# Kernel optimization log

Measured on AMD Instinct MI355X. Metric: run time of the kernel, lower is better.

The kernel has to match this reference:

```python
import jax, jax.numpy as jnp
import numpy as np

B, L, F, H = 8, 1024, 1024, 16
D = F // H  # feat_head = 64
EPS = 1e-5


def setup_inputs() -> dict:
    key = jax.random.key(0)
    ks = jax.random.split(key, 12)
    s = 1.0 / np.sqrt(F)
    inp = {
        "q": jax.random.normal(ks[0], (B, L, F), jnp.float32),
        "k": jax.random.normal(ks[1], (B, L, F), jnp.float32),
        "v": jax.random.normal(ks[2], (B, L, F), jnp.float32),
        "Wq": jax.random.uniform(ks[3], (F, F), jnp.float32, -s, s),
        "bq": jax.random.uniform(ks[4], (F,), jnp.float32, -s, s),
        "Wk": jax.random.uniform(ks[5], (F, F), jnp.float32, -s, s),
        "bk": jax.random.uniform(ks[6], (F,), jnp.float32, -s, s),
        "Wv": jax.random.uniform(ks[7], (F, F), jnp.float32, -s, s),
        "bv": jax.random.uniform(ks[8], (F,), jnp.float32, -s, s),
        "Wf": jax.random.uniform(ks[9], (F, F), jnp.float32, -s, s),
        "bf": jax.random.uniform(ks[10], (F,), jnp.float32, -s, s),
        "gamma": jnp.ones((F,), jnp.float32),
        "beta": jnp.zeros((F,), jnp.float32),
    }
    return inp


def _split_heads(x):
    # (B, L, F) -> (B*H, L, D), matching reshape->transpose(1,2)->reshape
    return x.reshape(B, L, H, D).transpose(0, 2, 1, 3).reshape(B * H, L, D)


def reference(q, k, v, Wq, bq, Wk, bk, Wv, bv, Wf, bf, gamma, beta):
    residual = q
    qh = _split_heads(q @ Wq.T + bq)
    kh = _split_heads(k @ Wk.T + bk)
    vh = _split_heads(v @ Wv.T + bv)
    # scores: (B*H, L, L)
    scores = jnp.einsum('nqd,nkd->nqk', qh, kh) / np.sqrt(D)
    raw_att = jax.nn.softmax(scores, axis=-1)
    att = jnp.einsum('nqk,nkd->nqd', raw_att, vh)  # (B*H, L, D)
    # faithful to original output recombine: reshape(H, B, L, D).permute(1,2,0,3)
    att = att.reshape(H, B, L, D).transpose(1, 2, 0, 3).reshape(B, L, F)
    att = att @ Wf.T + bf
    # dropout in eval mode = identity; activation is None
    x = att + residual
    mu = jnp.mean(x, axis=-1, keepdims=True)
    var = jnp.mean(jnp.square(x - mu), axis=-1, keepdims=True)
    out = (x - mu) * jax.lax.rsqrt(var + EPS) * gamma + beta
    return out, raw_att
```

## Files before the change

### kernel.cpp

```cpp
#include <hip/hip_runtime.h>

#define BB 8
#define LL 1024
#define FF 1024
#define HH 16
#define DD 64
#define NBH 128

typedef __attribute__((ext_vector_type(8))) short bf16x8;
typedef __attribute__((ext_vector_type(4))) float f32x4;

#define GLD_LDS16(g, l)                                                        \
  __builtin_amdgcn_global_load_lds(                                            \
      (const __attribute__((address_space(1))) unsigned int*)(g),              \
      (__attribute__((address_space(3))) unsigned int*)(l), 16, 0, 0)

__device__ __forceinline__ unsigned short f2bf(float f) {
  unsigned int u = __float_as_uint(f);
  unsigned int r = u + 0x7fffu + ((u >> 16) & 1u);
  return (unsigned short)(r >> 16);
}

__global__ __launch_bounds__(256) void cvt3_kernel(const float* __restrict__ s0,
                                                   const float* __restrict__ s1,
                                                   const float* __restrict__ s2,
                                                   short* __restrict__ dst, int n4) {
  int z = blockIdx.y;
  const float* src = (z == 0) ? s0 : (z == 1) ? s1 : s2;
  int i = blockIdx.x * 256 + threadIdx.x;
  if (i >= n4) return;
  float4 v = ((const float4*)src)[i];
  short4 o;
  o.x = (short)f2bf(v.x); o.y = (short)f2bf(v.y);
  o.z = (short)f2bf(v.z); o.w = (short)f2bf(v.w);
  ((short4*)(dst + (size_t)z * n4 * 4))[i] = o;
}

__global__ __launch_bounds__(256) void cvt4_kernel(const float* __restrict__ s0,
                                                   const float* __restrict__ s1,
                                                   const float* __restrict__ s2,
                                                   const float* __restrict__ s3,
                                                   short* __restrict__ dst, int n4) {
  int z = blockIdx.y;
  const float* src = (z == 0) ? s0 : (z == 1) ? s1 : (z == 2) ? s2 : s3;
  int i = blockIdx.x * 256 + threadIdx.x;
  if (i >= n4) return;
  float4 v = ((const float4*)src)[i];
  short4 o;
  o.x = (short)f2bf(v.x); o.y = (short)f2bf(v.y);
  o.z = (short)f2bf(v.z); o.w = (short)f2bf(v.w);
  ((short4*)(dst + (size_t)z * n4 * 4))[i] = o;
}

__global__ __launch_bounds__(256) void proj_qkv(
    const short* __restrict__ Aall, const short* __restrict__ Wall,
    const float* __restrict__ bq, const float* __restrict__ bk,
    const float* __restrict__ bv, short* __restrict__ Dall) {
  const int o = blockIdx.x + (blockIdx.y << 6) + (blockIdx.z << 9);
  const int n = ((o & 7) * 192) + (o >> 3);
  const int z = n >> 9;
  const int r = n & 511;
  const int by = r & 7, bx = r >> 3;

  const short* A  = Aall + (size_t)z * (BB * LL * FF);
  const short* Bt = Wall + (size_t)z * (FF * FF);
  const float* bias = (z == 0) ? bq : (z == 1) ? bk : bv;
  short* dst = Dall + (size_t)z * ((size_t)NBH * LL * DD);
  const float scale = (z == 0) ? 0.125f * 1.44269504088896f : 1.0f;

  __shared__ __attribute__((aligned(16))) short LB[128 * 136];
  short* As = LB;
  short* Bs = LB + 128 * 64;

  const int tid = threadIdx.x;
  const int lane = tid & 63, w = tid >> 6;
  const int wr = w >> 1, wc = w & 1;
  const int row16 = lane & 15, kg = lane >> 4;
  const int m0 = bx * 128, n0 = by * 128;

  const f32x4 z4 = {0.f, 0.f, 0.f, 0.f};
  f32x4 acc[4][4];
  for (int i = 0; i < 4; ++i)
    for (int j = 0; j < 4; ++j) acc[i][j] = z4;

  for (int k0 = 0; k0 < FF; k0 += 64) {
#pragma unroll
    for (int rr = 0; rr < 4; ++rr) {
      int e8 = tid + rr * 256;
      int row = e8 >> 3, cs = ((e8 & 7) ^ (row & 7)) * 8;
      GLD_LDS16(A + (size_t)(m0 + row) * FF + k0 + cs, As + e8 * 8);
      GLD_LDS16(Bt + (size_t)(n0 + row) * FF + k0 + cs, Bs + e8 * 8);
    }
    __syncthreads();
#pragma unroll
    for (int kk2 = 0; kk2 < 2; ++kk2) {
      bf16x8 af[4], bfr[4];
#pragma unroll
      for (int i = 0; i < 4; ++i) {
        int ra = wr * 64 + i * 16 + row16;
        int rb = wc * 64 + i * 16 + row16;
        af[i]  = *(const bf16x8*)(As + ra * 64 + ((((kk2 << 2) | kg) ^ (ra & 7)) << 3));
        bfr[i] = *(const bf16x8*)(Bs + rb * 64 + ((((kk2 << 2) | kg) ^ (rb & 7)) << 3));
      }
#pragma unroll
      for (int i = 0; i < 4; ++i)
#pragma unroll
        for (int j = 0; j < 4; ++j)
          acc[i][j] = __builtin_amdgcn_mfma_f32_16x16x32_bf16(af[i], bfr[j], acc[i][j], 0, 0, 0);
    }
    __syncthreads();
  }

  const int z2 = (z == 2);
#pragma unroll
  for (int i = 0; i < 4; ++i) {
#pragma unroll
    for (int j = 0; j < 4; ++j) {
      int nl = wc * 64 + j * 16 + row16;
      float bn = bias[n0 + nl];
#pragma unroll
      for (int rr = 0; rr < 4; ++rr) {
        int ml = wr * 64 + i * 16 + kg * 4 + rr;
        float val = (acc[i][j][rr] + bn) * scale;
        int rrow = z2 ? nl : ml, ccol = z2 ? ml : nl;
        LB[rrow * 136 + ccol] = (short)f2bf(val);
      }
    }
  }
  __syncthreads();
  const int b = m0 >> 10;
  const int lbase = m0 & 1023;
#pragma unroll
  for (int rr = 0; rr < 8; ++rr) {
    int e = tid + rr * 256;
    int row = e >> 4, c8 = e & 15;
    uint4 val = *(const uint4*)(LB + row * 136 + c8 * 8);
    if (!z2) {
      int l = lbase + row;
      int h = (n0 + c8 * 8) >> 6, d = (c8 & 7) * 8;
      *(uint4*)(dst + (((size_t)(b * HH + h)) * LL + l) * DD + d) = val;
    } else {
      int h = (n0 + row) >> 6, d = (n0 + row) & 63;
      int l = lbase + c8 * 8;
      *(uint4*)(dst + (((size_t)(b * HH + h)) * DD + d) * LL + l) = val;
    }
  }
}

__global__ __launch_bounds__(256) void attn_kernel(
    const short* __restrict__ Qh, const short* __restrict__ Kh,
    const short* __restrict__ Vt, float* __restrict__ Patt,
    short* __restrict__ attb) {
  const int o = blockIdx.x + (blockIdx.y << 4);
  const int n = ((o & 7) << 8) + (o >> 3);
  const int bh = n >> 4;
  const int q0 = (n & 15) * 64;
  const int tid = threadIdx.x;
  const int lane = tid & 63, w = tid >> 6;
  const int row16 = lane & 15, kg = lane >> 4;

  __shared__ __attribute__((aligned(16))) short Qs[64 * 64];
  __shared__ __attribute__((aligned(16))) short Ks[2][64 * 64];
  __shared__ __attribute__((aligned(16))) short Vts[2][64 * 64];
  __shared__ __attribute__((aligned(16))) short PsT[4][16 * 64];

#define STAGE_K(tt, bb)                                                        \
  {                                                                            \
    int e8a = tid, rowa = e8a >> 3, c8a = (e8a & 7) ^ (rowa & 7);              \
    GLD_LDS16(Kh + ((size_t)bh * LL + (tt) * 64 + rowa) * DD + c8a * 8,        \
              &Ks[bb][e8a * 8]);                                               \
    int e8b = tid + 256, rowb = e8b >> 3, c8b = (e8b & 7) ^ (rowb & 7);        \
    GLD_LDS16(Kh + ((size_t)bh * LL + (tt) * 64 + rowb) * DD + c8b * 8,        \
              &Ks[bb][e8b * 8]);                                               \
  }
#define STAGE_V(tt, bb)                                                        \
  {                                                                            \
    int e8a = tid, rowa = e8a >> 3, c8a = (e8a & 7) ^ (rowa & 7);              \
    GLD_LDS16(Vt + ((size_t)bh * DD + rowa) * LL + (tt) * 64 + c8a * 8,        \
              &Vts[bb][e8a * 8]);                                              \
    int e8b = tid + 256, rowb = e8b >> 3, c8b = (e8b & 7) ^ (rowb & 7);        \
    GLD_LDS16(Vt + ((size_t)bh * DD + rowb) * LL + (tt) * 64 + c8b * 8,        \
              &Vts[bb][e8b * 8]);                                              \
  }

  {
    int e8a = tid, rowa = e8a >> 3, c8a = (e8a & 7) ^ (rowa & 7);
    GLD_LDS16(Qh + ((size_t)bh * LL + q0 + rowa) * DD + c8a * 8, Qs + e8a * 8);
    int e8b = tid + 256, rowb = e8b >> 3, c8b = (e8b & 7) ^ (rowb & 7);
    GLD_LDS16(Qh + ((size_t)bh * LL + q0 + rowb) * DD + c8b * 8, Qs + e8b * 8);
  }
  STAGE_K(0, 0);
  __syncthreads();
  const int qrow = w * 16 + row16;
  bf16x8 aq0 = *(const bf16x8*)(Qs + qrow * 64 + ((kg ^ (qrow & 7)) << 3));
  bf16x8 aq1 = *(const bf16x8*)(Qs + qrow * 64 + (((kg + 4) ^ (qrow & 7)) << 3));

  const f32x4 z4 = {0.f, 0.f, 0.f, 0.f};
  float lsum = 0.f;

  for (int t = 0; t < 16; ++t) {
    int cur = t & 1;
    if (t < 15) STAGE_K(t + 1, cur ^ 1);
    f32x4 s[4] = {z4, z4, z4, z4};
#pragma unroll
    for (int tt = 0; tt < 4; ++tt) {
      int krow = tt * 16 + row16;
      bf16x8 b0 = *(const bf16x8*)(&Ks[cur][krow * 64 + ((kg ^ (krow & 7)) << 3)]);
      bf16x8 b1 = *(const bf16x8*)(&Ks[cur][krow * 64 + (((kg + 4) ^ (krow & 7)) << 3)]);
      s[tt] = __builtin_amdgcn_mfma_f32_16x16x32_bf16(b0, aq0, s[tt], 0, 0, 0);
      s[tt] = __builtin_amdgcn_mfma_f32_16x16x32_bf16(b1, aq1, s[tt], 0, 0, 0);
    }
#pragma unroll
    for (int tt = 0; tt < 4; ++tt)
#pragma unroll
      for (int rr = 0; rr < 4; ++rr) lsum += exp2f(s[tt][rr]);
    __syncthreads();
  }
  lsum += __shfl_xor(lsum, 16);
  lsum += __shfl_xor(lsum, 32);
  const float lc = __log2f(lsum);

  f32x4 oT[4] = {z4, z4, z4, z4};

  STAGE_K(0, 0);
  STAGE_V(0, 0);
  __syncthreads();
  for (int t = 0; t < 16; ++t) {
    int cur = t & 1;
    if (t < 15) {
      STAGE_K(t + 1, cur ^ 1);
      STAGE_V(t + 1, cur ^ 1);
    }
    f32x4 s[4] = {z4, z4, z4, z4};
#pragma unroll
    for (int tt = 0; tt < 4; ++tt) {
      int krow = tt * 16 + row16;
      bf16x8 b0 = *(const bf16x8*)(&Ks[cur][krow * 64 + ((kg ^ (krow & 7)) << 3)]);
      bf16x8 b1 = *(const bf16x8*)(&Ks[cur][krow * 64 + (((kg + 4) ^ (krow & 7)) << 3)]);
      s[tt] = __builtin_amdgcn_mfma_f32_16x16x32_bf16(b0, aq0, s[tt], 0, 0, 0);
      s[tt] = __builtin_amdgcn_mfma_f32_16x16x32_bf16(b1, aq1, s[tt], 0, 0, 0);
    }
    const int qq = q0 + w * 16 + row16;
    const int k0 = t * 64;
#pragma unroll
    for (int tt = 0; tt < 4; ++tt) {
      f32x4 pv;
#pragma unroll
      for (int rr = 0; rr < 4; ++rr) pv[rr] = exp2f(s[tt][rr] - lc);
      __builtin_nontemporal_store(
          pv, (f32x4*)(Patt + ((size_t)bh * LL + qq) * LL + k0 + tt * 16 + kg * 4));
      short4 ps;
      ps.x = (short)f2bf(pv[0]); ps.y = (short)f2bf(pv[1]);
      ps.z = (short)f2bf(pv[2]); ps.w = (short)f2bf(pv[3]);
      int c = ((tt * 2 + (kg >> 1)) ^ (row16 & 7));
      *(short4*)(&PsT[w][row16 * 64 + c * 8 + (kg & 1) * 4]) = ps;
    }
    bf16x8 pb0 = *(const bf16x8*)(&PsT[w][row16 * 64 + ((kg ^ (row16 & 7)) << 3)]);
    bf16x8 pb1 = *(const bf16x8*)(&PsT[w][row16 * 64 + (((4 + kg) ^ (row16 & 7)) << 3)]);
#pragma unroll
    for (int td = 0; td < 4; ++td) {
      int trow = td * 16 + row16;
      bf16x8 v0 = *(const bf16x8*)(&Vts[cur][trow * 64 + ((kg ^ (trow & 7)) << 3)]);
      bf16x8 v1 = *(const bf16x8*)(&Vts[cur][trow * 64 + (((kg + 4) ^ (trow & 7)) << 3)]);
      oT[td] = __builtin_amdgcn_mfma_f32_16x16x32_bf16(v0, pb0, oT[td], 0, 0, 0);
      oT[td] = __builtin_amdgcn_mfma_f32_16x16x32_bf16(v1, pb1, oT[td], 0, 0, 0);
    }
    __syncthreads();
  }

  const int iblk = bh >> 3;
  const int jb = bh & 7;
  const int qq = q0 + w * 16 + row16;
#pragma unroll
  for (int td = 0; td < 4; ++td) {
    short4 ov;
    ov.x = (short)f2bf(oT[td][0]); ov.y = (short)f2bf(oT[td][1]);
    ov.z = (short)f2bf(oT[td][2]); ov.w = (short)f2bf(oT[td][3]);
    *(short4*)(attb + ((size_t)jb * LL + qq) * FF + iblk * 64 + td * 16 + kg * 4) = ov;
  }
#undef STAGE_K
#undef STAGE_V
}

__global__ __launch_bounds__(256) void proj_out(
    const short* __restrict__ A, const short* __restrict__ Bt,
    const float* __restrict__ bias, const float* __restrict__ resid,
    float* __restrict__ xb) {
  const int o = blockIdx.x + (blockIdx.y << 6);
  const int n = ((o & 7) << 6) + (o >> 3);
  const int by = n & 7, bx = n >> 3;

  __shared__ __attribute__((aligned(16))) short As[128 * 64];
  __shared__ __attribute__((aligned(16))) short Bs[128 * 64];

  const int tid = threadIdx.x;
  const int lane = tid & 63, w = tid >> 6;
  const int wr = w >> 1, wc = w & 1;
  const int row16 = lane & 15, kg = lane >> 4;
  const int m0 = bx * 128, n0 = by * 128;

  const f32x4 z4 = {0.f, 0.f, 0.f, 0.f};
  f32x4 acc[4][4];
  for (int i = 0; i < 4; ++i)
    for (int j = 0; j < 4; ++j) acc[i][j] = z4;

  for (int k0 = 0; k0 < FF; k0 += 64) {
#pragma unroll
    for (int rr = 0; rr < 4; ++rr) {
      int e8 = tid + rr * 256;
      int row = e8 >> 3, cs = ((e8 & 7) ^ (row & 7)) * 8;
      GLD_LDS16(A + (size_t)(m0 + row) * FF + k0 + cs, As + e8 * 8);
      GLD_LDS16(Bt + (size_t)(n0 + row) * FF + k0 + cs, Bs + e8 * 8);
    }
    __syncthreads();
#pragma unroll
    for (int kk2 = 0; kk2 < 2; ++kk2) {
      bf16x8 af[4], bfr[4];
#pragma unroll
      for (int i = 0; i < 4; ++i) {
        int ra = wr * 64 + i * 16 + row16;
        int rb = wc * 64 + i * 16 + row16;
        af[i]  = *(const bf16x8*)(As + ra * 64 + ((((kk2 << 2) | kg) ^ (ra & 7)) << 3));
        bfr[i] = *(const bf16x8*)(Bs + rb * 64 + ((((kk2 << 2) | kg) ^ (rb & 7)) << 3));
      }
#pragma unroll
      for (int i = 0; i < 4; ++i)
#pragma unroll
        for (int j = 0; j < 4; ++j)
          acc[i][j] = __builtin_amdgcn_mfma_f32_16x16x32_bf16(af[i], bfr[j], acc[i][j], 0, 0, 0);
    }
    __syncthreads();
  }

#pragma unroll
  for (int i = 0; i < 4; ++i) {
#pragma unroll
    for (int j = 0; j < 4; ++j) {
      int ncol = n0 + wc * 64 + j * 16 + row16;
      float bn = bias[ncol];
#pragma unroll
      for (int rr = 0; rr < 4; ++rr) {
        int m = m0 + wr * 64 + i * 16 + kg * 4 + rr;
        xb[(size_t)m * FF + ncol] = acc[i][j][rr] + bn + resid[(size_t)m * FF + ncol];
      }
    }
  }
}

__global__ __launch_bounds__(256) void ln_kernel(const float* __restrict__ xb,
                                                 const float* __restrict__ gamma,
                                                 const float* __restrict__ beta,
                                                 float* __restrict__ out) {
  const int row = blockIdx.x;
  const int tid = threadIdx.x;
  const float4 v = *(const float4*)(xb + (size_t)row * FF + tid * 4);
  float s = v.x + v.y + v.z + v.w;
  float s2 = v.x * v.x + v.y * v.y + v.z * v.z + v.w * v.w;
#pragma unroll
  for (int o = 1; o < 64; o <<= 1) {
    s += __shfl_xor(s, o);
    s2 += __shfl_xor(s2, o);
  }
  __shared__ float ss[4], ss2[4];
  int w = tid >> 6, lane = tid & 63;
  if (lane == 0) { ss[w] = s; ss2[w] = s2; }
  __syncthreads();
  s = ss[0] + ss[1] + ss[2] + ss[3];
  s2 = ss2[0] + ss2[1] + ss2[2] + ss2[3];
  float mu = s * (1.0f / 1024.0f);
  float var = s2 * (1.0f / 1024.0f) - mu * mu;
  float rs = rsqrtf(var + 1e-5f);
  float4 g = *(const float4*)(gamma + tid * 4);
  float4 be = *(const float4*)(beta + tid * 4);
  float4 o;
  o.x = (v.x - mu) * rs * g.x + be.x;
  o.y = (v.y - mu) * rs * g.y + be.y;
  o.z = (v.z - mu) * rs * g.z + be.z;
  o.w = (v.w - mu) * rs * g.w + be.w;
  *(float4*)(out + (size_t)row * FF + tid * 4) = o;
}

extern "C" void kernel_launch(void* const* d_in, const int* in_sizes, int n_in,
                              void* d_out, int out_size, void* d_ws, size_t ws_size,
                              hipStream_t stream) {
  const float* q  = (const float*)d_in[0];
  const float* k  = (const float*)d_in[1];
  const float* v  = (const float*)d_in[2];
  const float* Wq = (const float*)d_in[3];
  const float* bq = (const float*)d_in[4];
  const float* Wk = (const float*)d_in[5];
  const float* bk = (const float*)d_in[6];
  const float* Wv = (const float*)d_in[7];
  const float* bv = (const float*)d_in[8];
  const float* Wf = (const float*)d_in[9];
  const float* bf = (const float*)d_in[10];
  const float* gamma = (const float*)d_in[11];
  const float* beta  = (const float*)d_in[12];

  float* out = (float*)d_out;
  float* Patt = out + (size_t)BB * LL * FF;

  char* ws = (char*)d_ws;
  const size_t MB = (size_t)1 << 20;
  short* qb = (short*)(ws + 0 * MB);
  short* Wb = (short*)(ws + 48 * MB);
  short* Qh = (short*)(ws + 56 * MB);
  short* Kh = (short*)(ws + 72 * MB);
  short* Vt = (short*)(ws + 88 * MB);
  short* attb = qb;
  float* xb = (float*)(ws + 16 * MB);

  const int nAct4 = BB * LL * FF / 4;
  const int nW4 = FF * FF / 4;
  cvt3_kernel<<<dim3((nAct4 + 255) / 256, 3), 256, 0, stream>>>(q, k, v, qb, nAct4);
  cvt4_kernel<<<dim3((nW4 + 255) / 256, 4), 256, 0, stream>>>(Wq, Wk, Wv, Wf, Wb, nW4);

  proj_qkv<<<dim3(64, 8, 3), 256, 0, stream>>>(qb, Wb, bq, bk, bv, Qh);
  attn_kernel<<<dim3(16, 128), 256, 0, stream>>>(Qh, Kh, Vt, Patt, attb);
  proj_out<<<dim3(64, 8), 256, 0, stream>>>(attb, Wb + 3 * (size_t)FF * FF, bf, q, xb);
  ln_kernel<<<8192, 256, 0, stream>>>(xb, gamma, beta, out);
}
```

Measured before the change: 303.5 us.

## Triple-buffer K in softmax-sum pass and replace syncthreads with vmcnt-gated barriers

The first attention pass now prefetches K two tiles ahead, borrowing the V double buffer as a third K buffer. Both passes replace __syncthreads with explicit s_waitcnt vmcnt(N) plus s_barrier, so only the current tile's async LDS loads are awaited while the next tile's loads stay in flight. MFMA sections are wrapped in s_setprio to favour matrix issue across waves. This adds dependence on exact vmcnt accounting, including the nontemporal Patt stores counted in the second pass, which is fragile if the instruction order changes.

New measurement: 291.7 us. -3.9%, faster.

```diff
diff --git a/kernel.cpp b/kernel.cpp
--- a/kernel.cpp
+++ b/kernel.cpp
@@ -164,23 +164,27 @@
   __shared__ __attribute__((aligned(16))) short Vts[2][64 * 64];
   __shared__ __attribute__((aligned(16))) short PsT[4][16 * 64];
 
-#define STAGE_K(tt, bb)                                                        \
+  auto kbuf3 = [&](int i) -> short* {
+    return (i == 2) ? &Vts[0][0] : &Ks[i][0];
+  };
+
+#define STAGE_K(tt, dstp)                                                      \
   {                                                                            \
     int e8a = tid, rowa = e8a >> 3, c8a = (e8a & 7) ^ (rowa & 7);              \
     GLD_LDS16(Kh + ((size_t)bh * LL + (tt) * 64 + rowa) * DD + c8a * 8,        \
-              &Ks[bb][e8a * 8]);                                               \
+              (dstp) + e8a * 8);                                               \
     int e8b = tid + 256, rowb = e8b >> 3, c8b = (e8b & 7) ^ (rowb & 7);        \
     GLD_LDS16(Kh + ((size_t)bh * LL + (tt) * 64 + rowb) * DD + c8b * 8,        \
-              &Ks[bb][e8b * 8]);                                               \
-  }
-#define STAGE_V(tt, bb)                                                        \
+              (dstp) + e8b * 8);                                               \
+  }
+#define STAGE_V(tt, dstp)                                                      \
   {                                                                            \
     int e8a = tid, rowa = e8a >> 3, c8a = (e8a & 7) ^ (rowa & 7);              \
     GLD_LDS16(Vt + ((size_t)bh * DD + rowa) * LL + (tt) * 64 + c8a * 8,        \
-              &Vts[bb][e8a * 8]);                                              \
+              (dstp) + e8a * 8);                                               \
     int e8b = tid + 256, rowb = e8b >> 3, c8b = (e8b & 7) ^ (rowb & 7);        \
     GLD_LDS16(Vt + ((size_t)bh * DD + rowb) * LL + (tt) * 64 + c8b * 8,        \
-              &Vts[bb][e8b * 8]);                                              \
+              (dstp) + e8b * 8);                                               \
   }
 
   {
@@ -189,8 +193,11 @@
     int e8b = tid + 256, rowb = e8b >> 3, c8b = (e8b & 7) ^ (rowb & 7);
     GLD_LDS16(Qh + ((size_t)bh * LL + q0 + rowb) * DD + c8b * 8, Qs + e8b * 8);
   }
-  STAGE_K(0, 0);
-  __syncthreads();
+  STAGE_K(0, kbuf3(0));
+  STAGE_K(1, kbuf3(1));
+  asm volatile("s_waitcnt vmcnt(2)" ::: "memory");
+  __builtin_amdgcn_s_barrier();
+
   const int qrow = w * 16 + row16;
   bf16x8 aq0 = *(const bf16x8*)(Qs + qrow * 64 + ((kg ^ (qrow & 7)) << 3));
   bf16x8 aq1 = *(const bf16x8*)(Qs + qrow * 64 + (((kg + 4) ^ (qrow & 7)) << 3));
@@ -199,9 +206,51 @@
   float lsum = 0.f;
 
   for (int t = 0; t < 16; ++t) {
-    int cur = t & 1;
-    if (t < 15) STAGE_K(t + 1, cur ^ 1);
+    const short* kb = kbuf3(t % 3);
+    if (t < 14) {
+      short* kd = kbuf3((t + 2) % 3);
+      STAGE_K(t + 2, kd);
+    }
     f32x4 s[4] = {z4, z4, z4, z4};
+    __builtin_amdgcn_s_setprio(1);
+#pragma unroll
+    for (int tt = 0; tt < 4; ++tt) {
+      int krow = tt * 16 + row16;
+      bf16x8 b0 = *(const bf16x8*)(kb + krow * 64 + ((kg ^ (krow & 7)) << 3));
+      bf16x8 b1 = *(const bf16x8*)(kb + krow * 64 + (((kg + 4) ^ (krow & 7)) << 3));
+      s[tt] = __builtin_amdgcn_mfma_f32_16x16x32_bf16(b0, aq0, s[tt], 0, 0, 0);
+      s[tt] = __builtin_amdgcn_mfma_f32_16x16x32_bf16(b1, aq1, s[tt], 0, 0, 0);
+    }
+    __builtin_amdgcn_s_setprio(0);
+#pragma unroll
+    for (int tt = 0; tt < 4; ++tt)
+#pragma unroll
+      for (int rr = 0; rr < 4; ++rr) lsum += exp2f(s[tt][rr]);
+    if (t < 14) {
+      asm volatile("s_waitcnt vmcnt(2)" ::: "memory");
+    } else {
+      asm volatile("s_waitcnt vmcnt(0)" ::: "memory");
+    }
+    __builtin_amdgcn_s_barrier();
+  }
+  lsum += __shfl_xor(lsum, 16);
+  lsum += __shfl_xor(lsum, 32);
+  const float lc = __log2f(lsum);
+
+  f32x4 oT[4] = {z4, z4, z4, z4};
+
+  STAGE_K(0, &Ks[0][0]);
+  STAGE_V(0, &Vts[0][0]);
+  asm volatile("s_waitcnt vmcnt(0)" ::: "memory");
+  __builtin_amdgcn_s_barrier();
+  for (int t = 0; t < 16; ++t) {
+    const int cur = t & 1;
+    if (t < 15) {
+      STAGE_K(t + 1, &Ks[cur ^ 1][0]);
+      STAGE_V(t + 1, &Vts[cur ^ 1][0]);
+    }
+    f32x4 s[4] = {z4, z4, z4, z4};
+    __builtin_amdgcn_s_setprio(1);
 #pragma unroll
     for (int tt = 0; tt < 4; ++tt) {
       int krow = tt * 16 + row16;
@@ -210,36 +259,7 @@
       s[tt] = __builtin_amdgcn_mfma_f32_16x16x32_bf16(b0, aq0, s[tt], 0, 0, 0);
       s[tt] = __builtin_amdgcn_mfma_f32_16x16x32_bf16(b1, aq1, s[tt], 0, 0, 0);
     }
-#pragma unroll
-    for (int tt = 0; tt < 4; ++tt)
-#pragma unroll
-      for (int rr = 0; rr < 4; ++rr) lsum += exp2f(s[tt][rr]);
-    __syncthreads();
-  }
-  lsum += __shfl_xor(lsum, 16);
-  lsum += __shfl_xor(lsum, 32);
-  const float lc = __log2f(lsum);
-
-  f32x4 oT[4] = {z4, z4, z4, z4};
-
-  STAGE_K(0, 0);
-  STAGE_V(0, 0);
-  __syncthreads();
-  for (int t = 0; t < 16; ++t) {
-    int cur = t & 1;
-    if (t < 15) {
-      STAGE_K(t + 1, cur ^ 1);
-      STAGE_V(t + 1, cur ^ 1);
-    }
-    f32x4 s[4] = {z4, z4, z4, z4};
-#pragma unroll
-    for (int tt = 0; tt < 4; ++tt) {
-      int krow = tt * 16 + row16;
-      bf16x8 b0 = *(const bf16x8*)(&Ks[cur][krow * 64 + ((kg ^ (krow & 7)) << 3)]);
-      bf16x8 b1 = *(const bf16x8*)(&Ks[cur][krow * 64 + (((kg + 4) ^ (krow & 7)) << 3)]);
-      s[tt] = __builtin_amdgcn_mfma_f32_16x16x32_bf16(b0, aq0, s[tt], 0, 0, 0);
-      s[tt] = __builtin_amdgcn_mfma_f32_16x16x32_bf16(b1, aq1, s[tt], 0, 0, 0);
-    }
+    __builtin_amdgcn_s_setprio(0);
     const int qq = q0 + w * 16 + row16;
     const int k0 = t * 64;
 #pragma unroll
@@ -257,6 +277,7 @@
     }
     bf16x8 pb0 = *(const bf16x8*)(&PsT[w][row16 * 64 + ((kg ^ (row16 & 7)) << 3)]);
     bf16x8 pb1 = *(const bf16x8*)(&PsT[w][row16 * 64 + (((4 + kg) ^ (row16 & 7)) << 3)]);
+    __builtin_amdgcn_s_setprio(1);
 #pragma unroll
     for (int td = 0; td < 4; ++td) {
       int trow = td * 16 + row16;
@@ -265,7 +286,11 @@
       oT[td] = __builtin_amdgcn_mfma_f32_16x16x32_bf16(v0, pb0, oT[td], 0, 0, 0);
       oT[td] = __builtin_amdgcn_mfma_f32_16x16x32_bf16(v1, pb1, oT[td], 0, 0, 0);
     }
-    __syncthreads();
+    __builtin_amdgcn_s_setprio(0);
+    if (t < 15) {
+      asm volatile("s_waitcnt vmcnt(4)" ::: "memory");
+      __builtin_amdgcn_s_barrier();
+    }
   }
 
   const int iblk = bh >> 3;
```
